# Optimization experiments

Measured on AMD Instinct MI355X. Metric: run time of the kernel, lower is better.

## Reference

```python
import jax, jax.numpy as jnp
import numpy as np

D_IN = 1024
D_OUT = 1024
N = 4096


def setup_inputs() -> dict:
    key = jax.random.key(0)
    ks = jax.random.split(key, 7)
    s_in = 1.0 / np.sqrt(D_IN)
    return {
        "x": jax.random.normal(ks[0], (N, D_IN), dtype=jnp.float32),
        "W_q": jax.random.uniform(ks[1], (D_IN, D_OUT), jnp.float32, -s_in, s_in),
        "b_q": jax.random.uniform(ks[2], (D_OUT,), jnp.float32, -s_in, s_in),
        "W_k": jax.random.uniform(ks[3], (D_IN, D_OUT), jnp.float32, -s_in, s_in),
        "b_k": jax.random.uniform(ks[4], (D_OUT,), jnp.float32, -s_in, s_in),
        "W_v": jax.random.uniform(ks[5], (D_IN, D_OUT), jnp.float32, -s_in, s_in),
        "b_v": jax.random.uniform(ks[6], (D_OUT,), jnp.float32, -s_in, s_in),
    }


def reference(x, W_q, b_q, W_k, b_k, W_v, b_v):
    # QKV projections (Linear with bias): [N, d_out]
    q = x @ W_q + b_q
    k = x @ W_k + b_k
    v = x @ W_v + b_v
    # Full attention: scores [N, N], scaled by sqrt(d_out)
    scores = (q @ k.T) / jnp.sqrt(jnp.asarray(k.shape[-1], q.dtype))
    attn = jax.nn.softmax(scores, axis=-1)
    return attn @ v  # [N, d_out]
```

## Files before the change

kernel.cpp:

```cpp
#include <hip/hip_runtime.h>

typedef __attribute__((ext_vector_type(8))) short short8;
typedef __attribute__((ext_vector_type(4))) float f32x4;
typedef __attribute__((ext_vector_type(8))) unsigned short ushort8;

typedef const unsigned int __attribute__((address_space(1)))* gas1_t;
typedef unsigned int __attribute__((address_space(3)))* las3_t;

__device__ __forceinline__ void gload_lds16(const void* g, void* l) {
  __builtin_amdgcn_global_load_lds((gas1_t)g, (las3_t)l, 16, 0, 0);
}

__device__ __forceinline__ unsigned short f2bf(float f) {
  unsigned int u = __float_as_uint(f);
  u += 0x7FFFu + ((u >> 16) & 1u);
  return (unsigned short)(u >> 16);
}
__device__ __forceinline__ float bf2f(unsigned short b) {
  return __uint_as_float(((unsigned int)b) << 16);
}

__global__ __launch_bounds__(256) void conv_f32_bf16(const float* __restrict__ in,
                                                     unsigned short* __restrict__ out, int n8) {
  int i = blockIdx.x * 256 + threadIdx.x;
  if (i >= n8) return;
  const f32x4* p = (const f32x4*)(in + (size_t)i * 8);
  f32x4 a = p[0], b = p[1];
  ushort8 o;
  o[0]=f2bf(a[0]); o[1]=f2bf(a[1]); o[2]=f2bf(a[2]); o[3]=f2bf(a[3]);
  o[4]=f2bf(b[0]); o[5]=f2bf(b[1]); o[6]=f2bf(b[2]); o[7]=f2bf(b[3]);
  *(ushort8*)(out + (size_t)i * 8) = o;
}

__global__ __launch_bounds__(256) void transconv_w(const float* __restrict__ Wq,
                                                   const float* __restrict__ Wk,
                                                   const float* __restrict__ Wv,
                                                   unsigned short* __restrict__ out) {
  __shared__ unsigned short tile[64][66];
  const float* W = (blockIdx.z == 0) ? Wq : ((blockIdx.z == 1) ? Wk : Wv);
  unsigned short* O = out + (size_t)blockIdx.z * 1048576;
  const int bi = blockIdx.x * 64;
  const int bo = blockIdx.y * 64;
#pragma unroll
  for (int p = 0; p < 16; ++p) {
    int idx = p * 256 + threadIdx.x;
    int r = idx >> 6, c = idx & 63;
    tile[r][c] = f2bf(W[(size_t)(bi + r) * 1024 + bo + c]);
  }
  __syncthreads();
#pragma unroll
  for (int p = 0; p < 16; ++p) {
    int idx = p * 256 + threadIdx.x;
    int r = idx >> 6, c = idx & 63;
    O[(size_t)(bo + r) * 1024 + bi + c] = tile[c][r];
  }
}

__global__ __launch_bounds__(256) void trans_bf16(const unsigned short* __restrict__ in,
                                                  unsigned short* __restrict__ out, int R, int C) {
  __shared__ unsigned short tile[64][66];
  const int br = blockIdx.x * 64, bc = blockIdx.y * 64;
#pragma unroll
  for (int p = 0; p < 16; ++p) {
    int idx = p * 256 + threadIdx.x;
    int r = idx >> 6, c = idx & 63;
    tile[r][c] = in[(size_t)(br + r) * C + bc + c];
  }
  __syncthreads();
#pragma unroll
  for (int p = 0; p < 16; ++p) {
    int idx = p * 256 + threadIdx.x;
    int r = idx >> 6, c = idx & 63;
    out[(size_t)(bc + r) * R + br + c] = tile[c][r];
  }
}

__global__ __launch_bounds__(256) void reduce_pv(const unsigned short* __restrict__ P,
                                                 const float* __restrict__ rsum,
                                                 float* __restrict__ out) {
  int i = blockIdx.x * 256 + threadIdx.x;
  const int m = (i * 8) >> 10;
  const float inv = 1.0f / rsum[m];
  float s[8] = {0.f, 0.f, 0.f, 0.f, 0.f, 0.f, 0.f, 0.f};
#pragma unroll
  for (int z = 0; z < 4; ++z) {
    ushort8 v = *(const ushort8*)(P + (size_t)z * 4194304 + (size_t)i * 8);
#pragma unroll
    for (int j = 0; j < 8; ++j) s[j] += bf2f(v[j]);
  }
  f32x4 o0, o1;
#pragma unroll
  for (int j = 0; j < 4; ++j) { o0[j] = s[j] * inv; o1[j] = s[4 + j] * inv; }
  f32x4* po = (f32x4*)(out + (size_t)i * 8);
  po[0] = o0; po[1] = o1;
}

template <int BM, int BN, int MI, int NI, int EPI>
__global__ __launch_bounds__(256, 2) void gemm_bt(
    const unsigned short* __restrict__ A, const unsigned short* __restrict__ B,
    int lda, int ldb, int K, void* __restrict__ C, int ldc,
    size_t strideBz, size_t strideCz,
    const float* __restrict__ bq, const float* __restrict__ bk, const float* __restrict__ bv,
    float scale, float* __restrict__ rsum) {
  static_assert(BM == 2 * MI * 16 && BN == 2 * NI * 16, "tile mismatch");
  __shared__ unsigned short As[2][BM * 32];
  __shared__ unsigned short Bs[2][BN * 32];
  const int tid = threadIdx.x;
  const int lane = tid & 63;
  const int w = tid >> 6;
  const int wr = w >> 1, wc = w & 1;

  const int nwgx = gridDim.x;
  const int nwg = nwgx * gridDim.y;
  const int lin = blockIdx.y * nwgx + blockIdx.x;
  const int swz = (lin & 7) * (nwg >> 3) + (lin >> 3);
  const int m0 = (swz / nwgx) * BM;
  const int n0 = (swz % nwgx) * BN;
  const int z = blockIdx.z;
  const unsigned short* Bz = B + (size_t)z * strideBz;
  const size_t koff = (EPI == 2) ? (size_t)z * K : 0;

  f32x4 acc[MI][NI];
#pragma unroll
  for (int i = 0; i < MI; ++i)
#pragma unroll
    for (int j = 0; j < NI; ++j) acc[i][j] = f32x4{0.f, 0.f, 0.f, 0.f};

  const int l16 = lane & 15;
  const int kh = (lane >> 4) << 3;

  const unsigned short* aptr[BM / 64];
  const unsigned short* bptr[BN / 64];
#pragma unroll
  for (int i = 0; i < BM / 64; ++i) {
    int t = i * 256 + tid;
    aptr[i] = A + (size_t)(m0 + (t >> 2)) * lda + koff + (t & 3) * 8;
  }
#pragma unroll
  for (int i = 0; i < BN / 64; ++i) {
    int t = i * 256 + tid;
    bptr[i] = Bz + (size_t)(n0 + (t >> 2)) * ldb + koff + (t & 3) * 8;
  }

#define STAGE(buf, k0)                                                        \
  do {                                                                        \
    _Pragma("unroll") for (int _si = 0; _si < BM / 64; ++_si) {               \
      const int _st = _si * 256 + tid;                                        \
      gload_lds16(aptr[_si] + (k0), &As[buf][_st * 8]);                       \
    }                                                                         \
    _Pragma("unroll") for (int _si = 0; _si < BN / 64; ++_si) {               \
      const int _st = _si * 256 + tid;                                        \
      gload_lds16(bptr[_si] + (k0), &Bs[buf][_st * 8]);                       \
    }                                                                         \
  } while (0)

  STAGE(0, 0);
  __syncthreads();

  const int NT = K / 32;
  for (int t = 0; t < NT; ++t) {
    const int cur = t & 1;
    if (t + 1 < NT) STAGE(cur ^ 1, (t + 1) * 32);
    short8 a[MI], b[NI];
#pragma unroll
    for (int mi = 0; mi < MI; ++mi)
      a[mi] = *(const short8*)(&As[cur][(wr * (MI * 16) + mi * 16 + l16) * 32 + kh]);
#pragma unroll
    for (int ni = 0; ni < NI; ++ni)
      b[ni] = *(const short8*)(&Bs[cur][(wc * (NI * 16) + ni * 16 + l16) * 32 + kh]);
#pragma unroll
    for (int mi = 0; mi < MI; ++mi)
#pragma unroll
      for (int ni = 0; ni < NI; ++ni)
        acc[mi][ni] = __builtin_amdgcn_mfma_f32_16x16x32_bf16(a[mi], b[ni], acc[mi][ni], 0, 0, 0);
    __syncthreads();
  }
#undef STAGE

  const int row0 = m0 + wr * (MI * 16) + ((lane >> 4) << 2);
  const int col0 = n0 + wc * (NI * 16);

  if constexpr (EPI == 0) {
    unsigned short* O = (unsigned short*)C + (size_t)z * strideCz;
    const float* bias = (z == 0) ? bq : ((z == 1) ? bk : bv);
#pragma unroll
    for (int mi = 0; mi < MI; ++mi)
#pragma unroll
      for (int ni = 0; ni < NI; ++ni) {
        const int col = col0 + ni * 16 + l16;
        const int row = row0 + mi * 16;
        float bvv = bias[col];
#pragma unroll
        for (int r = 0; r < 4; ++r)
          O[(size_t)(row + r) * ldc + col] = f2bf(acc[mi][ni][r] + bvv);
      }
  } else if constexpr (EPI == 1) {
    unsigned short* O = (unsigned short*)C;
#pragma unroll
    for (int mi = 0; mi < MI; ++mi) {
      float rs[4] = {0.f, 0.f, 0.f, 0.f};
      const int row = row0 + mi * 16;
#pragma unroll
      for (int ni = 0; ni < NI; ++ni) {
        const int col = col0 + ni * 16 + l16;
#pragma unroll
        for (int r = 0; r < 4; ++r) {
          unsigned short ub = f2bf(__expf(acc[mi][ni][r] * scale));
          O[(size_t)(row + r) * ldc + col] = ub;
          rs[r] += bf2f(ub);
        }
      }
#pragma unroll
      for (int off = 1; off <= 8; off <<= 1) {
#pragma unroll
        for (int r = 0; r < 4; ++r) rs[r] += __shfl_xor(rs[r], off);
      }
      if (l16 == 0) {
#pragma unroll
        for (int r = 0; r < 4; ++r) unsafeAtomicAdd(&rsum[row + r], rs[r]);
      }
    }
  } else {
    unsigned short* O = (unsigned short*)C + (size_t)z * strideCz;
#pragma unroll
    for (int mi = 0; mi < MI; ++mi)
#pragma unroll
      for (int ni = 0; ni < NI; ++ni) {
        const int col = col0 + ni * 16 + l16;
        const int row = row0 + mi * 16;
#pragma unroll
        for (int r = 0; r < 4; ++r)
          O[(size_t)(row + r) * ldc + col] = f2bf(acc[mi][ni][r]);
      }
  }
}

extern "C" void kernel_launch(void* const* d_in, const int* in_sizes, int n_in,
                              void* d_out, int out_size, void* d_ws, size_t ws_size,
                              hipStream_t stream) {
  const float* x  = (const float*)d_in[0];
  const float* Wq = (const float*)d_in[1];
  const float* bq = (const float*)d_in[2];
  const float* Wk = (const float*)d_in[3];
  const float* bk = (const float*)d_in[4];
  const float* Wv = (const float*)d_in[5];
  const float* bv = (const float*)d_in[6];
  float* out = (float*)d_out;
  char* ws = (char*)d_ws;
  const size_t MB = 1024 * 1024;

  unsigned short* xb  = (unsigned short*)(ws + 0);
  unsigned short* wt  = (unsigned short*)(ws + 8 * MB);
  unsigned short* qkv = (unsigned short*)(ws + 14 * MB);
  unsigned short* qb  = qkv;
  unsigned short* kb  = qkv + (size_t)4194304;
  unsigned short* vb  = qkv + (size_t)2 * 4194304;
  float*          rsum= (float*)(ws + 37 * MB);
  unsigned short* vt  = (unsigned short*)(ws + 38 * MB);
  unsigned short* S   = (unsigned short*)(ws + 46 * MB);
  unsigned short* P   = (unsigned short*)(ws + 0);

  conv_f32_bf16<<<2048, 256, 0, stream>>>(x, xb, 524288);
  transconv_w<<<dim3(16, 16, 3), 256, 0, stream>>>(Wq, Wk, Wv, wt);
  gemm_bt<128, 128, 4, 4, 0><<<dim3(8, 32, 3), 256, 0, stream>>>(
      xb, wt, 1024, 1024, 1024, qkv, 1024,
      (size_t)1048576, (size_t)4194304, bq, bk, bv, 1.0f, nullptr);
  trans_bf16<<<dim3(64, 16), 256, 0, stream>>>(vb, vt, 4096, 1024);
  hipMemsetAsync(rsum, 0, 4096 * sizeof(float), stream);
  gemm_bt<128, 128, 4, 4, 1><<<dim3(32, 32), 256, 0, stream>>>(
      qb, kb, 1024, 1024, 1024, S, 4096,
      (size_t)0, (size_t)0, nullptr, nullptr, nullptr, 0.03125f, rsum);
  gemm_bt<128, 128, 4, 4, 2><<<dim3(8, 32, 4), 256, 0, stream>>>(
      S, vt, 4096, 4096, 1024, P, 1024,
      (size_t)0, (size_t)4194304, nullptr, nullptr, nullptr, 1.0f, nullptr);
  reduce_pv<<<2048, 256, 0, stream>>>(P, rsum, out);
}
```

Measured before the change: 150.9 us.

## Replace 128x128 GEMM with 256x256 tile, 512 threads, XOR-swizzled LDS, deeper prefetch

All three GEMMs move from a 128x128x32 tile with 256 threads to a 256x256x64 tile with 8 waves. Each wave computes a 128x64 sub-tile. The LDS layout uses an XOR swizzle on 16-byte chunks to avoid bank conflicts. Loads are prefetched two stages ahead, with explicit vmcnt waits and raw s_barrier instead of __syncthreads. This raises arithmetic intensity per tile and overlaps loads with MFMA, at the cost of far fewer workgroups (e.g. 192 for QKV, 256 for QK^T), which risks underfilling the CUs, and higher register pressure from 128 accumulator floats per lane.

```diff
diff --git a/kernel.cpp b/kernel.cpp
--- a/kernel.cpp
+++ b/kernel.cpp
@@ -95,98 +95,115 @@
   po[0] = o0; po[1] = o1;
 }
 
-template <int BM, int BN, int MI, int NI, int EPI>
-__global__ __launch_bounds__(256, 2) void gemm_bt(
+template <int EPI>
+__global__ __launch_bounds__(512, 1) void gemm256(
     const unsigned short* __restrict__ A, const unsigned short* __restrict__ B,
     int lda, int ldb, int K, void* __restrict__ C, int ldc,
     size_t strideBz, size_t strideCz,
     const float* __restrict__ bq, const float* __restrict__ bk, const float* __restrict__ bv,
     float scale, float* __restrict__ rsum) {
-  static_assert(BM == 2 * MI * 16 && BN == 2 * NI * 16, "tile mismatch");
-  __shared__ unsigned short As[2][BM * 32];
-  __shared__ unsigned short Bs[2][BN * 32];
+  __shared__ unsigned short As[2][2][8192];
+  __shared__ unsigned short Bs[2][2][8192];
   const int tid = threadIdx.x;
   const int lane = tid & 63;
   const int w = tid >> 6;
-  const int wr = w >> 1, wc = w & 1;
+  const int wr = w >> 2;
+  const int wc = w & 3;
+  const int l16 = lane & 15;
+  const int q = lane >> 4;
 
   const int nwgx = gridDim.x;
   const int nwg = nwgx * gridDim.y;
   const int lin = blockIdx.y * nwgx + blockIdx.x;
   const int swz = (lin & 7) * (nwg >> 3) + (lin >> 3);
-  const int m0 = (swz / nwgx) * BM;
-  const int n0 = (swz % nwgx) * BN;
+  const int m0 = (swz / nwgx) * 256;
+  const int n0 = (swz % nwgx) * 256;
   const int z = blockIdx.z;
   const unsigned short* Bz = B + (size_t)z * strideBz;
   const size_t koff = (EPI == 2) ? (size_t)z * K : 0;
 
-  f32x4 acc[MI][NI];
-#pragma unroll
-  for (int i = 0; i < MI; ++i)
-#pragma unroll
-    for (int j = 0; j < NI; ++j) acc[i][j] = f32x4{0.f, 0.f, 0.f, 0.f};
-
-  const int l16 = lane & 15;
-  const int kh = (lane >> 4) << 3;
-
-  const unsigned short* aptr[BM / 64];
-  const unsigned short* bptr[BN / 64];
-#pragma unroll
-  for (int i = 0; i < BM / 64; ++i) {
-    int t = i * 256 + tid;
-    aptr[i] = A + (size_t)(m0 + (t >> 2)) * lda + koff + (t & 3) * 8;
-  }
-#pragma unroll
-  for (int i = 0; i < BN / 64; ++i) {
-    int t = i * 256 + tid;
-    bptr[i] = Bz + (size_t)(n0 + (t >> 2)) * ldb + koff + (t & 3) * 8;
-  }
-
-#define STAGE(buf, k0)                                                        \
+  f32x4 acc[8][4];
+#pragma unroll
+  for (int i = 0; i < 8; ++i)
+#pragma unroll
+    for (int j = 0; j < 4; ++j) acc[i][j] = f32x4{0.f, 0.f, 0.f, 0.f};
+
+  const unsigned short* ap[2][2];
+  const unsigned short* bp[2][2];
+#pragma unroll
+  for (int h = 0; h < 2; ++h)
+#pragma unroll
+    for (int j = 0; j < 2; ++j) {
+      const int g = (j << 9) + tid;
+      const int row = g >> 3;
+      const int cb = (g & 7) ^ (row & 7);
+      ap[h][j] = A + (size_t)(m0 + h * 128 + row) * lda + koff + cb * 8;
+      bp[h][j] = Bz + (size_t)(n0 + h * 128 + row) * ldb + koff + cb * 8;
+    }
+
+#define STG(buf, k0)                                                          \
   do {                                                                        \
-    _Pragma("unroll") for (int _si = 0; _si < BM / 64; ++_si) {               \
-      const int _st = _si * 256 + tid;                                        \
-      gload_lds16(aptr[_si] + (k0), &As[buf][_st * 8]);                       \
-    }                                                                         \
-    _Pragma("unroll") for (int _si = 0; _si < BN / 64; ++_si) {               \
-      const int _st = _si * 256 + tid;                                        \
-      gload_lds16(bptr[_si] + (k0), &Bs[buf][_st * 8]);                       \
+    _Pragma("unroll") for (int _h = 0; _h < 2; ++_h) {                        \
+      _Pragma("unroll") for (int _j = 0; _j < 2; ++_j) {                      \
+        gload_lds16(ap[_h][_j] + (k0), &As[buf][_h][((_j << 9) + tid) * 8]);  \
+        gload_lds16(bp[_h][_j] + (k0), &Bs[buf][_h][((_j << 9) + tid) * 8]);  \
+      }                                                                       \
     }                                                                         \
   } while (0)
 
-  STAGE(0, 0);
-  __syncthreads();
-
-  const int NT = K / 32;
+  const int NT = K / 64;
+  STG(0, 0);
+  STG(1, 64);
+
   for (int t = 0; t < NT; ++t) {
     const int cur = t & 1;
-    if (t + 1 < NT) STAGE(cur ^ 1, (t + 1) * 32);
-    short8 a[MI], b[NI];
-#pragma unroll
-    for (int mi = 0; mi < MI; ++mi)
-      a[mi] = *(const short8*)(&As[cur][(wr * (MI * 16) + mi * 16 + l16) * 32 + kh]);
-#pragma unroll
-    for (int ni = 0; ni < NI; ++ni)
-      b[ni] = *(const short8*)(&Bs[cur][(wc * (NI * 16) + ni * 16 + l16) * 32 + kh]);
-#pragma unroll
-    for (int mi = 0; mi < MI; ++mi)
-#pragma unroll
-      for (int ni = 0; ni < NI; ++ni)
-        acc[mi][ni] = __builtin_amdgcn_mfma_f32_16x16x32_bf16(a[mi], b[ni], acc[mi][ni], 0, 0, 0);
-    __syncthreads();
-  }
-#undef STAGE
-
-  const int row0 = m0 + wr * (MI * 16) + ((lane >> 4) << 2);
-  const int col0 = n0 + wc * (NI * 16);
+    if (t + 1 < NT) {
+      asm volatile("s_waitcnt vmcnt(8)" ::: "memory");
+    } else {
+      asm volatile("s_waitcnt vmcnt(0)" ::: "memory");
+    }
+    __builtin_amdgcn_sched_barrier(0);
+    __builtin_amdgcn_s_barrier();
+    __builtin_amdgcn_sched_barrier(0);
+
+#pragma unroll
+    for (int ks = 0; ks < 2; ++ks) {
+      const int sw = ((ks << 2) + q) ^ (l16 & 7);
+      short8 bfr[4], afr[8];
+#pragma unroll
+      for (int ni = 0; ni < 4; ++ni) {
+        const int r = ((wc & 1) << 6) + ni * 16 + l16;
+        bfr[ni] = *(const short8*)(&Bs[cur][wc >> 1][r * 64 + sw * 8]);
+      }
+#pragma unroll
+      for (int mi = 0; mi < 8; ++mi) {
+        const int r = mi * 16 + l16;
+        afr[mi] = *(const short8*)(&As[cur][wr][r * 64 + sw * 8]);
+      }
+#pragma unroll
+      for (int mi = 0; mi < 8; ++mi)
+#pragma unroll
+        for (int ni = 0; ni < 4; ++ni)
+          acc[mi][ni] = __builtin_amdgcn_mfma_f32_16x16x32_bf16(afr[mi], bfr[ni], acc[mi][ni], 0, 0, 0);
+    }
+
+    __builtin_amdgcn_sched_barrier(0);
+    __builtin_amdgcn_s_barrier();
+    __builtin_amdgcn_sched_barrier(0);
+    if (t + 2 < NT) STG(cur, (t + 2) * 64);
+  }
+#undef STG
+
+  const int row0 = m0 + wr * 128 + q * 4;
+  const int col0 = n0 + wc * 64;
 
   if constexpr (EPI == 0) {
     unsigned short* O = (unsigned short*)C + (size_t)z * strideCz;
     const float* bias = (z == 0) ? bq : ((z == 1) ? bk : bv);
 #pragma unroll
-    for (int mi = 0; mi < MI; ++mi)
-#pragma unroll
-      for (int ni = 0; ni < NI; ++ni) {
+    for (int mi = 0; mi < 8; ++mi)
+#pragma unroll
+      for (int ni = 0; ni < 4; ++ni) {
         const int col = col0 + ni * 16 + l16;
         const int row = row0 + mi * 16;
         float bvv = bias[col];
@@ -197,11 +214,11 @@
   } else if constexpr (EPI == 1) {
     unsigned short* O = (unsigned short*)C;
 #pragma unroll
-    for (int mi = 0; mi < MI; ++mi) {
+    for (int mi = 0; mi < 8; ++mi) {
       float rs[4] = {0.f, 0.f, 0.f, 0.f};
       const int row = row0 + mi * 16;
 #pragma unroll
-      for (int ni = 0; ni < NI; ++ni) {
+      for (int ni = 0; ni < 4; ++ni) {
         const int col = col0 + ni * 16 + l16;
 #pragma unroll
         for (int r = 0; r < 4; ++r) {
@@ -223,9 +240,9 @@
   } else {
     unsigned short* O = (unsigned short*)C + (size_t)z * strideCz;
 #pragma unroll
-    for (int mi = 0; mi < MI; ++mi)
-#pragma unroll
-      for (int ni = 0; ni < NI; ++ni) {
+    for (int mi = 0; mi < 8; ++mi)
+#pragma unroll
+      for (int ni = 0; ni < 4; ++ni) {
         const int col = col0 + ni * 16 + l16;
         const int row = row0 + mi * 16;
 #pragma unroll
@@ -262,15 +279,15 @@
 
   conv_f32_bf16<<<2048, 256, 0, stream>>>(x, xb, 524288);
   transconv_w<<<dim3(16, 16, 3), 256, 0, stream>>>(Wq, Wk, Wv, wt);
-  gemm_bt<128, 128, 4, 4, 0><<<dim3(8, 32, 3), 256, 0, stream>>>(
+  gemm256<0><<<dim3(4, 16, 3), 512, 0, stream>>>(
       xb, wt, 1024, 1024, 1024, qkv, 1024,
       (size_t)1048576, (size_t)4194304, bq, bk, bv, 1.0f, nullptr);
   trans_bf16<<<dim3(64, 16), 256, 0, stream>>>(vb, vt, 4096, 1024);
   hipMemsetAsync(rsum, 0, 4096 * sizeof(float), stream);
-  gemm_bt<128, 128, 4, 4, 1><<<dim3(32, 32), 256, 0, stream>>>(
+  gemm256<1><<<dim3(16, 16), 512, 0, stream>>>(
       qb, kb, 1024, 1024, 1024, S, 4096,
       (size_t)0, (size_t)0, nullptr, nullptr, nullptr, 0.03125f, rsum);
-  gemm_bt<128, 128, 4, 4, 2><<<dim3(8, 32, 4), 256, 0, stream>>>(
+  gemm256<2><<<dim3(4, 16, 4), 512, 0, stream>>>(
       S, vt, 4096, 4096, 1024, P, 1024,
       (size_t)0, (size_t)4194304, nullptr, nullptr, nullptr, 1.0f, nullptr);
   reduce_pv<<<2048, 256, 0, stream>>>(P, rsum, out);
```

Result: slower. 156.0 us (+3.4%).

## Switch GEMMs to 32x32x16 MFMA with XOR-swizzled LDS layout

Applied to the files above, without the earlier changes.

Replaces the 16x16x32 bf16 MFMA tiles with 32x32x16 MFMA tiles (each wave computes 2x2 tiles of 32x32 over two k-substeps) and rewrites the epilogues for the 32x32 accumulator layout. It also XOR-swizzles the 16-byte chunks in LDS by row to reduce bank conflicts on the fragment reads. The larger MFMA halves the number of LDS fragment loads per flop and uses a denser instruction. The trade-off is an epilogue with strided stores and more shuffles for the row sums.

```diff
diff --git a/kernel.cpp b/kernel.cpp
--- a/kernel.cpp
+++ b/kernel.cpp
@@ -2,6 +2,7 @@
 
 typedef __attribute__((ext_vector_type(8))) short short8;
 typedef __attribute__((ext_vector_type(4))) float f32x4;
+typedef __attribute__((ext_vector_type(16))) float f32x16;
 typedef __attribute__((ext_vector_type(8))) unsigned short ushort8;
 
 typedef const unsigned int __attribute__((address_space(1)))* gas1_t;
@@ -102,13 +103,15 @@
     size_t strideBz, size_t strideCz,
     const float* __restrict__ bq, const float* __restrict__ bk, const float* __restrict__ bv,
     float scale, float* __restrict__ rsum) {
-  static_assert(BM == 2 * MI * 16 && BN == 2 * NI * 16, "tile mismatch");
+  static_assert(BM == 2 * MI * 32 && BN == 2 * NI * 32, "tile mismatch");
   __shared__ unsigned short As[2][BM * 32];
   __shared__ unsigned short Bs[2][BN * 32];
   const int tid = threadIdx.x;
   const int lane = tid & 63;
   const int w = tid >> 6;
   const int wr = w >> 1, wc = w & 1;
+  const int l32 = lane & 31;
+  const int kq = lane >> 5;
 
   const int nwgx = gridDim.x;
   const int nwg = nwgx * gridDim.y;
@@ -120,26 +123,27 @@
   const unsigned short* Bz = B + (size_t)z * strideBz;
   const size_t koff = (EPI == 2) ? (size_t)z * K : 0;
 
-  f32x4 acc[MI][NI];
+  f32x16 acc[MI][NI];
 #pragma unroll
   for (int i = 0; i < MI; ++i)
 #pragma unroll
-    for (int j = 0; j < NI; ++j) acc[i][j] = f32x4{0.f, 0.f, 0.f, 0.f};
-
-  const int l16 = lane & 15;
-  const int kh = (lane >> 4) << 3;
+    for (int j = 0; j < NI; ++j)
+#pragma unroll
+      for (int e = 0; e < 16; ++e) acc[i][j][e] = 0.f;
 
   const unsigned short* aptr[BM / 64];
   const unsigned short* bptr[BN / 64];
 #pragma unroll
   for (int i = 0; i < BM / 64; ++i) {
     int t = i * 256 + tid;
-    aptr[i] = A + (size_t)(m0 + (t >> 2)) * lda + koff + (t & 3) * 8;
+    int r = t >> 2;
+    aptr[i] = A + (size_t)(m0 + r) * lda + koff + ((t & 3) ^ (r & 3)) * 8;
   }
 #pragma unroll
   for (int i = 0; i < BN / 64; ++i) {
     int t = i * 256 + tid;
-    bptr[i] = Bz + (size_t)(n0 + (t >> 2)) * ldb + koff + (t & 3) * 8;
+    int r = t >> 2;
+    bptr[i] = Bz + (size_t)(n0 + r) * ldb + koff + ((t & 3) ^ (r & 3)) * 8;
   }
 
 #define STAGE(buf, k0)                                                        \
@@ -161,24 +165,34 @@
   for (int t = 0; t < NT; ++t) {
     const int cur = t & 1;
     if (t + 1 < NT) STAGE(cur ^ 1, (t + 1) * 32);
-    short8 a[MI], b[NI];
-#pragma unroll
-    for (int mi = 0; mi < MI; ++mi)
-      a[mi] = *(const short8*)(&As[cur][(wr * (MI * 16) + mi * 16 + l16) * 32 + kh]);
-#pragma unroll
-    for (int ni = 0; ni < NI; ++ni)
-      b[ni] = *(const short8*)(&Bs[cur][(wc * (NI * 16) + ni * 16 + l16) * 32 + kh]);
-#pragma unroll
-    for (int mi = 0; mi < MI; ++mi)
-#pragma unroll
-      for (int ni = 0; ni < NI; ++ni)
-        acc[mi][ni] = __builtin_amdgcn_mfma_f32_16x16x32_bf16(a[mi], b[ni], acc[mi][ni], 0, 0, 0);
+    short8 a[2][MI], b[2][NI];
+#pragma unroll
+    for (int ks = 0; ks < 2; ++ks) {
+#pragma unroll
+      for (int mi = 0; mi < MI; ++mi) {
+        const int r = wr * (MI * 32) + mi * 32 + l32;
+        a[ks][mi] = *(const short8*)(&As[cur][r * 32 + (((ks << 1) + kq) ^ (r & 3)) * 8]);
+      }
+#pragma unroll
+      for (int ni = 0; ni < NI; ++ni) {
+        const int r = wc * (NI * 32) + ni * 32 + l32;
+        b[ks][ni] = *(const short8*)(&Bs[cur][r * 32 + (((ks << 1) + kq) ^ (r & 3)) * 8]);
+      }
+    }
+#pragma unroll
+    for (int ks = 0; ks < 2; ++ks)
+#pragma unroll
+      for (int mi = 0; mi < MI; ++mi)
+#pragma unroll
+        for (int ni = 0; ni < NI; ++ni)
+          acc[mi][ni] = __builtin_amdgcn_mfma_f32_32x32x16_bf16(
+              a[ks][mi], b[ks][ni], acc[mi][ni], 0, 0, 0);
     __syncthreads();
   }
 #undef STAGE
 
-  const int row0 = m0 + wr * (MI * 16) + ((lane >> 4) << 2);
-  const int col0 = n0 + wc * (NI * 16);
+  const int row00 = m0 + wr * (MI * 32) + 4 * kq;
+  const int col00 = n0 + wc * (NI * 32);
 
   if constexpr (EPI == 0) {
     unsigned short* O = (unsigned short*)C + (size_t)z * strideCz;
@@ -187,37 +201,43 @@
     for (int mi = 0; mi < MI; ++mi)
 #pragma unroll
       for (int ni = 0; ni < NI; ++ni) {
-        const int col = col0 + ni * 16 + l16;
-        const int row = row0 + mi * 16;
-        float bvv = bias[col];
-#pragma unroll
-        for (int r = 0; r < 4; ++r)
-          O[(size_t)(row + r) * ldc + col] = f2bf(acc[mi][ni][r] + bvv);
+        const int col = col00 + ni * 32 + l32;
+        const float bvv = bias[col];
+#pragma unroll
+        for (int j = 0; j < 16; ++j) {
+          const int row = row00 + mi * 32 + (j & 3) + 8 * (j >> 2);
+          O[(size_t)row * ldc + col] = f2bf(acc[mi][ni][j] + bvv);
+        }
       }
   } else if constexpr (EPI == 1) {
     unsigned short* O = (unsigned short*)C;
 #pragma unroll
     for (int mi = 0; mi < MI; ++mi) {
-      float rs[4] = {0.f, 0.f, 0.f, 0.f};
-      const int row = row0 + mi * 16;
-#pragma unroll
-      for (int ni = 0; ni < NI; ++ni) {
-        const int col = col0 + ni * 16 + l16;
-#pragma unroll
-        for (int r = 0; r < 4; ++r) {
-          unsigned short ub = f2bf(__expf(acc[mi][ni][r] * scale));
-          O[(size_t)(row + r) * ldc + col] = ub;
-          rs[r] += bf2f(ub);
-        }
-      }
-#pragma unroll
-      for (int off = 1; off <= 8; off <<= 1) {
-#pragma unroll
-        for (int r = 0; r < 4; ++r) rs[r] += __shfl_xor(rs[r], off);
-      }
-      if (l16 == 0) {
-#pragma unroll
-        for (int r = 0; r < 4; ++r) unsafeAtomicAdd(&rsum[row + r], rs[r]);
+      float rs[16];
+#pragma unroll
+      for (int j = 0; j < 16; ++j) rs[j] = 0.f;
+#pragma unroll
+      for (int ni = 0; ni < NI; ++ni) {
+        const int col = col00 + ni * 32 + l32;
+#pragma unroll
+        for (int j = 0; j < 16; ++j) {
+          const int row = row00 + mi * 32 + (j & 3) + 8 * (j >> 2);
+          unsigned short ub = f2bf(__expf(acc[mi][ni][j] * scale));
+          O[(size_t)row * ldc + col] = ub;
+          rs[j] += bf2f(ub);
+        }
+      }
+#pragma unroll
+      for (int off = 1; off <= 16; off <<= 1) {
+#pragma unroll
+        for (int j = 0; j < 16; ++j) rs[j] += __shfl_xor(rs[j], off);
+      }
+      if (l32 == 0) {
+#pragma unroll
+        for (int j = 0; j < 16; ++j) {
+          const int row = row00 + mi * 32 + (j & 3) + 8 * (j >> 2);
+          unsafeAtomicAdd(&rsum[row], rs[j]);
+        }
       }
     }
   } else {
@@ -226,11 +246,12 @@
     for (int mi = 0; mi < MI; ++mi)
 #pragma unroll
       for (int ni = 0; ni < NI; ++ni) {
-        const int col = col0 + ni * 16 + l16;
-        const int row = row0 + mi * 16;
-#pragma unroll
-        for (int r = 0; r < 4; ++r)
-          O[(size_t)(row + r) * ldc + col] = f2bf(acc[mi][ni][r]);
+        const int col = col00 + ni * 32 + l32;
+#pragma unroll
+        for (int j = 0; j < 16; ++j) {
+          const int row = row00 + mi * 32 + (j & 3) + 8 * (j >> 2);
+          O[(size_t)row * ldc + col] = f2bf(acc[mi][ni][j]);
+        }
       }
   }
 }
@@ -262,15 +283,15 @@
 
   conv_f32_bf16<<<2048, 256, 0, stream>>>(x, xb, 524288);
   transconv_w<<<dim3(16, 16, 3), 256, 0, stream>>>(Wq, Wk, Wv, wt);
-  gemm_bt<128, 128, 4, 4, 0><<<dim3(8, 32, 3), 256, 0, stream>>>(
+  gemm_bt<128, 128, 2, 2, 0><<<dim3(8, 32, 3), 256, 0, stream>>>(
       xb, wt, 1024, 1024, 1024, qkv, 1024,
       (size_t)1048576, (size_t)4194304, bq, bk, bv, 1.0f, nullptr);
   trans_bf16<<<dim3(64, 16), 256, 0, stream>>>(vb, vt, 4096, 1024);
   hipMemsetAsync(rsum, 0, 4096 * sizeof(float), stream);
-  gemm_bt<128, 128, 4, 4, 1><<<dim3(32, 32), 256, 0, stream>>>(
+  gemm_bt<128, 128, 2, 2, 1><<<dim3(32, 32), 256, 0, stream>>>(
       qb, kb, 1024, 1024, 1024, S, 4096,
       (size_t)0, (size_t)0, nullptr, nullptr, nullptr, 0.03125f, rsum);
-  gemm_bt<128, 128, 4, 4, 2><<<dim3(8, 32, 4), 256, 0, stream>>>(
+  gemm_bt<128, 128, 2, 2, 2><<<dim3(8, 32, 4), 256, 0, stream>>>(
       S, vt, 4096, 4096, 1024, P, 1024,
       (size_t)0, (size_t)4194304, nullptr, nullptr, nullptr, 1.0f, nullptr);
   reduce_pv<<<2048, 256, 0, stream>>>(P, rsum, out);
```

Result: slower. 179.0 us (+18.6%).
